# Optimization experiments

Measured on AMD Instinct MI355X. Metric: run time of the kernel, lower is better.

Reference implementation:

```python
import jax, jax.numpy as jnp
import numpy as np

B, T, I, H, G = 4096, 1024, 1, 16, 48  # G = 3*H gates

def _gru_layer(inp, w_ih, w_hh, b_ih, b_hh):
    # inp: [B, T, Din] -> out: [B, T, H]. PyTorch GRU gate math.
    # Precompute all input-side gate projections once (batched GEMM).
    xg = jnp.einsum('btd,gd->tbg', inp, w_ih) + b_ih  # [T, B, 3H]

    def step(h, xg_t):
        hg = h @ w_hh.T + b_hh                         # [B, 3H]
        xr, xz, xn = jnp.split(xg_t, 3, axis=-1)
        hr, hz, hn = jnp.split(hg, 3, axis=-1)
        r = jax.nn.sigmoid(xr + hr)
        z = jax.nn.sigmoid(xz + hz)
        n = jnp.tanh(xn + r * hn)
        h_new = (1.0 - z) * n + z * h
        return h_new, h_new

    h0 = jnp.zeros((inp.shape[0], H), dtype=inp.dtype)
    _, ys = jax.lax.scan(step, h0, xg)                 # ys: [T, B, H]
    return jnp.transpose(ys, (1, 0, 2))                # [B, T, H]

def setup_inputs() -> dict:
    key = jax.random.key(0)
    ks = jax.random.split(key, 8)
    s = 1.0 / np.sqrt(H)  # PyTorch default uniform(-1/sqrt(H), 1/sqrt(H))
    u = lambda k, shape: jax.random.uniform(k, shape, jnp.float32, -s, s)
    return {
        'x':      jax.random.normal(ks[0], (B, T, I), jnp.float32),
        'w_ih0':  u(ks[1], (G, I)),
        'w_ih12': u(ks[2], (2, G, H)),
        'w_hh':   u(ks[3], (3, G, H)),
        'b_ih':   u(ks[4], (3, G)),
        'b_hh':   u(ks[5], (3, G)),
        'fc_w':   u(ks[6], (5, H)),
        'fc_b':   u(ks[7], (5,)),
    }

def reference(x, w_ih0, w_ih12, w_hh, b_ih, b_hh, fc_w, fc_b):
    # 3-layer GRU (dropout=0.3 between layers is identity in eval mode)
    h = _gru_layer(x, w_ih0,     w_hh[0], b_ih[0], b_hh[0])
    h = _gru_layer(h, w_ih12[0], w_hh[1], b_ih[1], b_hh[1])
    h = _gru_layer(h, w_ih12[1], w_hh[2], b_ih[2], b_hh[2])
    # Linear head on the last timestep
    return h[:, -1, :] @ fc_w.T + fc_b                 # [B, 5]
```

## Files before the change

kernel.cpp:

```cpp
#include <hip/hip_runtime.h>
#include <stdint.h>

#define TSTEPS 1024
#define L2E 1.4426950408889634f

typedef float v2f __attribute__((ext_vector_type(2)));
typedef float v4f __attribute__((ext_vector_type(4)));

__device__ __forceinline__ float rcpf_(float v) { return __builtin_amdgcn_rcpf(v); }
__device__ __forceinline__ float ex2(float v) { return __builtin_amdgcn_exp2f(v); }
#define PKFMA(a, b, c) __builtin_elementwise_fma((a), (b), (c))

__device__ __forceinline__ float dpp_x1(float v) {
    return __int_as_float(__builtin_amdgcn_update_dpp(
        0, __float_as_int(v), 0xB1, 0xF, 0xF, true));
}
__device__ __forceinline__ float pairsum(v2f a) {
    float s = a.x + a.y;
    return s + dpp_x1(s);
}

__device__ __forceinline__ v2f ldg2(const float* p) {
    v2f r; uint64_t a = (uint64_t)p;
    asm volatile("global_load_dwordx2 %0, %1, off\n\ts_waitcnt vmcnt(0)"
                 : "=v"(r) : "v"(a));
    return r;
}
__device__ __forceinline__ float ldg1(const float* p) {
    float r; uint64_t a = (uint64_t)p;
    asm volatile("global_load_dword %0, %1, off\n\ts_waitcnt vmcnt(0)"
                 : "=v"(r) : "v"(a));
    return r;
}

__global__ __launch_bounds__(256, 2) void gru3_pair(
    const float* __restrict__ x,
    const float* __restrict__ w_ih0,
    const float* __restrict__ w_ih12,
    const float* __restrict__ w_hh,
    const float* __restrict__ b_ih,
    const float* __restrict__ b_hh,
    const float* __restrict__ fc_w,
    const float* __restrict__ fc_b,
    float* __restrict__ out)
{
    __shared__ float xs[8][TSTEPS];
    __shared__ float hb[8][4][16];

    const int l31 = threadIdx.x & 31;
    const int grp = threadIdx.x >> 5;
    const int u = l31 >> 1;
    const int c = l31 & 1;
    const int c8 = c * 8;
    const int seq = blockIdx.x * 8 + grp;

    {
        const float4* xg = (const float4*)(x + (size_t)blockIdx.x * 8 * TSTEPS);
        float4* xs4 = (float4*)&xs[0][0];
#pragma unroll
        for (int j = 0; j < 8; ++j)
            xs4[threadIdx.x + 256 * j] = xg[threadIdx.x + 256 * j];
        ((float*)hb)[threadIdx.x] = 0.f;
        ((float*)hb)[256 + threadIdx.x] = 0.f;
    }

    const float qs[3] = {-L2E, -L2E, 2.f * L2E};
    v2f wh[3][3][4];
    v2f wi[2][3][4];
#pragma unroll
    for (int l = 0; l < 3; ++l)
#pragma unroll
        for (int q = 0; q < 3; ++q)
#pragma unroll
            for (int m = 0; m < 4; ++m)
                wh[l][q][m] =
                    ldg2(w_hh + (l * 48 + q * 16 + u) * 16 + c8 + 2 * m) * qs[q];
#pragma unroll
    for (int l = 0; l < 2; ++l)
#pragma unroll
        for (int q = 0; q < 3; ++q)
#pragma unroll
            for (int m = 0; m < 4; ++m)
                wi[l][q][m] =
                    ldg2(w_ih12 + (l * 48 + q * 16 + u) * 16 + c8 + 2 * m) * qs[q];

    v2f bir[3], biz[3], binh[3], binx[2];
#pragma unroll
    for (int l = 0; l < 3; ++l) {
        float vr = -(ldg1(b_ih + l * 48 + u) + ldg1(b_hh + l * 48 + u)) * L2E;
        float vz = -(ldg1(b_ih + l * 48 + 16 + u) + ldg1(b_hh + l * 48 + 16 + u)) * L2E;
        float vn = ldg1(b_hh + l * 48 + 32 + u) * (2.f * L2E);
        bir[l] = (v2f){c ? 0.f : vr, 0.f};
        biz[l] = (v2f){c ? 0.f : vz, 0.f};
        binh[l] = (v2f){c ? 0.f : vn, 0.f};
    }
#pragma unroll
    for (int l = 0; l < 2; ++l) {
        float vx = ldg1(b_ih + (l + 1) * 48 + 32 + u) * (2.f * L2E);
        binx[l] = (v2f){c ? 0.f : vx, 0.f};
    }
    const float bnx0 = ldg1(b_ih + 32 + u) * (2.f * L2E);
    const float wxr = ldg1(w_ih0 + u) * -L2E;
    const float wxz = ldg1(w_ih0 + 16 + u) * -L2E;
    const float wxn = ldg1(w_ih0 + 32 + u) * (2.f * L2E);

    __syncthreads();

    v2f h0s[4], h1s[4], h2s[4];
#pragma unroll
    for (int m = 0; m < 4; ++m) {
        h0s[m] = (v2f){0.f, 0.f};
        h1s[m] = (v2f){0.f, 0.f};
        h2s[m] = (v2f){0.f, 0.f};
    }
    float h0o = 0.f, h1o = 0.f, h2o = 0.f;

    const float* xrow = &xs[grp][0];
    float* hw0 = &hb[grp][0][u];
    float* hw1 = &hb[grp][1][u];
    float* hw2 = &hb[grp][2][u];
    const float* hr0 = &hb[grp][0][c8];
    const float* hr1 = &hb[grp][1][c8];
    const float* hr2 = &hb[grp][2][c8];

#define RD4(dst, p)                                                       \
    do {                                                                  \
        v4f ta = *(const v4f*)(p);                                        \
        v4f tb = *(const v4f*)((p) + 4);                                  \
        dst[0] = __builtin_shufflevector(ta, ta, 0, 1);                   \
        dst[1] = __builtin_shufflevector(ta, ta, 2, 3);                   \
        dst[2] = __builtin_shufflevector(tb, tb, 0, 1);                   \
        dst[3] = __builtin_shufflevector(tb, tb, 2, 3);                   \
    } while (0)

    auto step = [&](bool F0, bool F1, bool F2, int t0) {
        v2f a;
        if (F0) {
            float xt = xrow[t0];
            a = PKFMA(wh[0][0][0], h0s[0], bir[0]);
            a = PKFMA(wh[0][0][1], h0s[1], a);
            a = PKFMA(wh[0][0][2], h0s[2], a);
            a = PKFMA(wh[0][0][3], h0s[3], a);
            float sr = fmaf(wxr, xt, pairsum(a));
            a = PKFMA(wh[0][1][0], h0s[0], biz[0]);
            a = PKFMA(wh[0][1][1], h0s[1], a);
            a = PKFMA(wh[0][1][2], h0s[2], a);
            a = PKFMA(wh[0][1][3], h0s[3], a);
            float sz = fmaf(wxz, xt, pairsum(a));
            a = PKFMA(wh[0][2][0], h0s[0], binh[0]);
            a = PKFMA(wh[0][2][1], h0s[1], a);
            a = PKFMA(wh[0][2][2], h0s[2], a);
            a = PKFMA(wh[0][2][3], h0s[3], a);
            float sn = pairsum(a);
            float r = rcpf_(1.f + ex2(sr));
            float z = rcpf_(1.f + ex2(sz));
            float ut = fmaf(r, sn, fmaf(wxn, xt, bnx0));
            float n = fmaf(-2.f, rcpf_(ex2(ut) + 1.f), 1.f);
            h0o = fmaf(z, h0o - n, n);
        }
        if (F1) {
            a = PKFMA(wh[1][0][0], h1s[0], bir[1]);
            a = PKFMA(wh[1][0][1], h1s[1], a);
            a = PKFMA(wh[1][0][2], h1s[2], a);
            a = PKFMA(wh[1][0][3], h1s[3], a);
            a = PKFMA(wi[0][0][0], h0s[0], a);
            a = PKFMA(wi[0][0][1], h0s[1], a);
            a = PKFMA(wi[0][0][2], h0s[2], a);
            a = PKFMA(wi[0][0][3], h0s[3], a);
            float sr = pairsum(a);
            a = PKFMA(wh[1][1][0], h1s[0], biz[1]);
            a = PKFMA(wh[1][1][1], h1s[1], a);
            a = PKFMA(wh[1][1][2], h1s[2], a);
            a = PKFMA(wh[1][1][3], h1s[3], a);
            a = PKFMA(wi[0][1][0], h0s[0], a);
            a = PKFMA(wi[0][1][1], h0s[1], a);
            a = PKFMA(wi[0][1][2], h0s[2], a);
            a = PKFMA(wi[0][1][3], h0s[3], a);
            float sz = pairsum(a);
            a = PKFMA(wh[1][2][0], h1s[0], binh[1]);
            a = PKFMA(wh[1][2][1], h1s[1], a);
            a = PKFMA(wh[1][2][2], h1s[2], a);
            a = PKFMA(wh[1][2][3], h1s[3], a);
            float snh = pairsum(a);
            a = PKFMA(wi[0][2][0], h0s[0], binx[0]);
            a = PKFMA(wi[0][2][1], h0s[1], a);
            a = PKFMA(wi[0][2][2], h0s[2], a);
            a = PKFMA(wi[0][2][3], h0s[3], a);
            float snx = pairsum(a);
            float r = rcpf_(1.f + ex2(sr));
            float z = rcpf_(1.f + ex2(sz));
            float ut = fmaf(r, snh, snx);
            float n = fmaf(-2.f, rcpf_(ex2(ut) + 1.f), 1.f);
            h1o = fmaf(z, h1o - n, n);
        }
        if (F2) {
            a = PKFMA(wh[2][0][0], h2s[0], bir[2]);
            a = PKFMA(wh[2][0][1], h2s[1], a);
            a = PKFMA(wh[2][0][2], h2s[2], a);
            a = PKFMA(wh[2][0][3], h2s[3], a);
            a = PKFMA(wi[1][0][0], h1s[0], a);
            a = PKFMA(wi[1][0][1], h1s[1], a);
            a = PKFMA(wi[1][0][2], h1s[2], a);
            a = PKFMA(wi[1][0][3], h1s[3], a);
            float sr = pairsum(a);
            a = PKFMA(wh[2][1][0], h2s[0], biz[2]);
            a = PKFMA(wh[2][1][1], h2s[1], a);
            a = PKFMA(wh[2][1][2], h2s[2], a);
            a = PKFMA(wh[2][1][3], h2s[3], a);
            a = PKFMA(wi[1][1][0], h1s[0], a);
            a = PKFMA(wi[1][1][1], h1s[1], a);
            a = PKFMA(wi[1][1][2], h1s[2], a);
            a = PKFMA(wi[1][1][3], h1s[3], a);
            float sz = pairsum(a);
            a = PKFMA(wh[2][2][0], h2s[0], binh[2]);
            a = PKFMA(wh[2][2][1], h2s[1], a);
            a = PKFMA(wh[2][2][2], h2s[2], a);
            a = PKFMA(wh[2][2][3], h2s[3], a);
            float snh = pairsum(a);
            a = PKFMA(wi[1][2][0], h1s[0], binx[1]);
            a = PKFMA(wi[1][2][1], h1s[1], a);
            a = PKFMA(wi[1][2][2], h1s[2], a);
            a = PKFMA(wi[1][2][3], h1s[3], a);
            float snx = pairsum(a);
            float r = rcpf_(1.f + ex2(sr));
            float z = rcpf_(1.f + ex2(sz));
            float ut = fmaf(r, snh, snx);
            float n = fmaf(-2.f, rcpf_(ex2(ut) + 1.f), 1.f);
            h2o = fmaf(z, h2o - n, n);
        }
        if (F0) *hw0 = h0o;
        if (F1) *hw1 = h1o;
        if (F2) *hw2 = h2o;
        if (F0) RD4(h0s, hr0);
        if (F1) RD4(h1s, hr1);
        if (F2) RD4(h2s, hr2);
    };

    step(true, false, false, 0);
    step(true, true, false, 1);
#pragma unroll 2
    for (int t0 = 2; t0 < TSTEPS; ++t0) step(true, true, true, t0);
    step(false, true, true, 0);
    step(false, false, true, 0);

    if (l31 < 5) {
        float acc = fc_b[l31];
#pragma unroll
        for (int j = 0; j < 16; ++j)
            acc = fmaf(fc_w[l31 * 16 + j], hb[grp][2][j], acc);
        out[seq * 5 + l31] = acc;
    }
#undef RD4
}

extern "C" void kernel_launch(void* const* d_in, const int* in_sizes, int n_in,
                              void* d_out, int out_size, void* d_ws, size_t ws_size,
                              hipStream_t stream) {
    const float* x      = (const float*)d_in[0];
    const float* w_ih0  = (const float*)d_in[1];
    const float* w_ih12 = (const float*)d_in[2];
    const float* w_hh   = (const float*)d_in[3];
    const float* b_ih   = (const float*)d_in[4];
    const float* b_hh   = (const float*)d_in[5];
    const float* fc_w   = (const float*)d_in[6];
    const float* fc_b   = (const float*)d_in[7];
    float* out = (float*)d_out;

    gru3_pair<<<512, 256, 0, stream>>>(
        x, w_ih0, w_ih12, w_hh, b_ih, b_hh, fc_w, fc_b, out);
}
```

Before: 565.5 us.

## Double-buffer hidden states and split sigmoid work across lane pairs

```diff
diff --git a/kernel.cpp b/kernel.cpp
--- a/kernel.cpp
+++ b/kernel.cpp
@@ -33,7 +33,7 @@
     return r;
 }
 
-__global__ __launch_bounds__(256, 2) void gru3_pair(
+__global__ __launch_bounds__(256, 2) void gru3_pipe(
     const float* __restrict__ x,
     const float* __restrict__ w_ih0,
     const float* __restrict__ w_ih12,
@@ -106,12 +106,12 @@
 
     __syncthreads();
 
-    v2f h0s[4], h1s[4], h2s[4];
+    v2f hA0[4], hA1[4], hA2[4], hB0[4], hB1[4], hB2[4];
 #pragma unroll
     for (int m = 0; m < 4; ++m) {
-        h0s[m] = (v2f){0.f, 0.f};
-        h1s[m] = (v2f){0.f, 0.f};
-        h2s[m] = (v2f){0.f, 0.f};
+        hA0[m] = (v2f){0.f, 0.f};
+        hA1[m] = (v2f){0.f, 0.f};
+        hA2[m] = (v2f){0.f, 0.f};
     }
     float h0o = 0.f, h1o = 0.f, h2o = 0.f;
 
@@ -133,115 +133,127 @@
         dst[3] = __builtin_shufflevector(tb, tb, 2, 3);                   \
     } while (0)
 
-    auto step = [&](bool F0, bool F1, bool F2, int t0) {
-        v2f a;
-        if (F0) {
-            float xt = xrow[t0];
-            a = PKFMA(wh[0][0][0], h0s[0], bir[0]);
-            a = PKFMA(wh[0][0][1], h0s[1], a);
-            a = PKFMA(wh[0][0][2], h0s[2], a);
-            a = PKFMA(wh[0][0][3], h0s[3], a);
-            float sr = fmaf(wxr, xt, pairsum(a));
-            a = PKFMA(wh[0][1][0], h0s[0], biz[0]);
-            a = PKFMA(wh[0][1][1], h0s[1], a);
-            a = PKFMA(wh[0][1][2], h0s[2], a);
-            a = PKFMA(wh[0][1][3], h0s[3], a);
-            float sz = fmaf(wxz, xt, pairsum(a));
-            a = PKFMA(wh[0][2][0], h0s[0], binh[0]);
-            a = PKFMA(wh[0][2][1], h0s[1], a);
-            a = PKFMA(wh[0][2][2], h0s[2], a);
-            a = PKFMA(wh[0][2][3], h0s[3], a);
-            float sn = pairsum(a);
-            float r = rcpf_(1.f + ex2(sr));
-            float z = rcpf_(1.f + ex2(sz));
-            float ut = fmaf(r, sn, fmaf(wxn, xt, bnx0));
-            float n = fmaf(-2.f, rcpf_(ex2(ut) + 1.f), 1.f);
-            h0o = fmaf(z, h0o - n, n);
-        }
-        if (F1) {
-            a = PKFMA(wh[1][0][0], h1s[0], bir[1]);
-            a = PKFMA(wh[1][0][1], h1s[1], a);
-            a = PKFMA(wh[1][0][2], h1s[2], a);
-            a = PKFMA(wh[1][0][3], h1s[3], a);
-            a = PKFMA(wi[0][0][0], h0s[0], a);
-            a = PKFMA(wi[0][0][1], h0s[1], a);
-            a = PKFMA(wi[0][0][2], h0s[2], a);
-            a = PKFMA(wi[0][0][3], h0s[3], a);
-            float sr = pairsum(a);
-            a = PKFMA(wh[1][1][0], h1s[0], biz[1]);
-            a = PKFMA(wh[1][1][1], h1s[1], a);
-            a = PKFMA(wh[1][1][2], h1s[2], a);
-            a = PKFMA(wh[1][1][3], h1s[3], a);
-            a = PKFMA(wi[0][1][0], h0s[0], a);
-            a = PKFMA(wi[0][1][1], h0s[1], a);
-            a = PKFMA(wi[0][1][2], h0s[2], a);
-            a = PKFMA(wi[0][1][3], h0s[3], a);
-            float sz = pairsum(a);
-            a = PKFMA(wh[1][2][0], h1s[0], binh[1]);
-            a = PKFMA(wh[1][2][1], h1s[1], a);
-            a = PKFMA(wh[1][2][2], h1s[2], a);
-            a = PKFMA(wh[1][2][3], h1s[3], a);
-            float snh = pairsum(a);
-            a = PKFMA(wi[0][2][0], h0s[0], binx[0]);
-            a = PKFMA(wi[0][2][1], h0s[1], a);
-            a = PKFMA(wi[0][2][2], h0s[2], a);
-            a = PKFMA(wi[0][2][3], h0s[3], a);
-            float snx = pairsum(a);
-            float r = rcpf_(1.f + ex2(sr));
-            float z = rcpf_(1.f + ex2(sz));
-            float ut = fmaf(r, snh, snx);
-            float n = fmaf(-2.f, rcpf_(ex2(ut) + 1.f), 1.f);
-            h1o = fmaf(z, h1o - n, n);
-        }
-        if (F2) {
-            a = PKFMA(wh[2][0][0], h2s[0], bir[2]);
-            a = PKFMA(wh[2][0][1], h2s[1], a);
-            a = PKFMA(wh[2][0][2], h2s[2], a);
-            a = PKFMA(wh[2][0][3], h2s[3], a);
-            a = PKFMA(wi[1][0][0], h1s[0], a);
-            a = PKFMA(wi[1][0][1], h1s[1], a);
-            a = PKFMA(wi[1][0][2], h1s[2], a);
-            a = PKFMA(wi[1][0][3], h1s[3], a);
-            float sr = pairsum(a);
-            a = PKFMA(wh[2][1][0], h2s[0], biz[2]);
-            a = PKFMA(wh[2][1][1], h2s[1], a);
-            a = PKFMA(wh[2][1][2], h2s[2], a);
-            a = PKFMA(wh[2][1][3], h2s[3], a);
-            a = PKFMA(wi[1][1][0], h1s[0], a);
-            a = PKFMA(wi[1][1][1], h1s[1], a);
-            a = PKFMA(wi[1][1][2], h1s[2], a);
-            a = PKFMA(wi[1][1][3], h1s[3], a);
-            float sz = pairsum(a);
-            a = PKFMA(wh[2][2][0], h2s[0], binh[2]);
-            a = PKFMA(wh[2][2][1], h2s[1], a);
-            a = PKFMA(wh[2][2][2], h2s[2], a);
-            a = PKFMA(wh[2][2][3], h2s[3], a);
-            float snh = pairsum(a);
-            a = PKFMA(wi[1][2][0], h1s[0], binx[1]);
-            a = PKFMA(wi[1][2][1], h1s[1], a);
-            a = PKFMA(wi[1][2][2], h1s[2], a);
-            a = PKFMA(wi[1][2][3], h1s[3], a);
-            float snx = pairsum(a);
-            float r = rcpf_(1.f + ex2(sr));
-            float z = rcpf_(1.f + ex2(sz));
-            float ut = fmaf(r, snh, snx);
-            float n = fmaf(-2.f, rcpf_(ex2(ut) + 1.f), 1.f);
-            h2o = fmaf(z, h2o - n, n);
-        }
-        if (F0) *hw0 = h0o;
-        if (F1) *hw1 = h1o;
-        if (F2) *hw2 = h2o;
-        if (F0) RD4(h0s, hr0);
-        if (F1) RD4(h1s, hr1);
-        if (F2) RD4(h2s, hr2);
-    };
-
-    step(true, false, false, 0);
-    step(true, true, false, 1);
-#pragma unroll 2
-    for (int t0 = 2; t0 < TSTEPS; ++t0) step(true, true, true, t0);
-    step(false, true, true, 0);
-    step(false, false, true, 0);
+#define STEP(I0, I1, I2, O0, O1, O2, F0, F1, F2, XT)                      \
+  do {                                                                    \
+    v2f a;                                                                \
+    if (F0) {                                                             \
+      a = PKFMA(wh[0][0][0], I0[0], bir[0]);                              \
+      a = PKFMA(wh[0][0][1], I0[1], a);                                   \
+      a = PKFMA(wh[0][0][2], I0[2], a);                                   \
+      a = PKFMA(wh[0][0][3], I0[3], a);                                   \
+      float sr = fmaf(wxr, (XT), pairsum(a));                             \
+      a = PKFMA(wh[0][1][0], I0[0], biz[0]);                              \
+      a = PKFMA(wh[0][1][1], I0[1], a);                                   \
+      a = PKFMA(wh[0][1][2], I0[2], a);                                   \
+      a = PKFMA(wh[0][1][3], I0[3], a);                                   \
+      float sz = fmaf(wxz, (XT), pairsum(a));                             \
+      a = PKFMA(wh[0][2][0], I0[0], binh[0]);                             \
+      a = PKFMA(wh[0][2][1], I0[1], a);                                   \
+      a = PKFMA(wh[0][2][2], I0[2], a);                                   \
+      a = PKFMA(wh[0][2][3], I0[3], a);                                   \
+      float sn = pairsum(a);                                              \
+      float p = c ? sz : sr;                                              \
+      float sg = rcpf_(1.f + ex2(p));                                     \
+      float og = dpp_x1(sg);                                              \
+      float r = c ? og : sg;                                              \
+      float z = c ? sg : og;                                              \
+      float ut = fmaf(r, sn, fmaf(wxn, (XT), bnx0));                      \
+      float n = fmaf(-2.f, rcpf_(ex2(ut) + 1.f), 1.f);                    \
+      h0o = fmaf(z, h0o - n, n);                                          \
+    }                                                                     \
+    *hw0 = h0o;                                                           \
+    RD4(O0, hr0);                                                         \
+    if (F1) {                                                             \
+      a = PKFMA(wh[1][0][0], I1[0], bir[1]);                              \
+      a = PKFMA(wh[1][0][1], I1[1], a);                                   \
+      a = PKFMA(wh[1][0][2], I1[2], a);                                   \
+      a = PKFMA(wh[1][0][3], I1[3], a);                                   \
+      a = PKFMA(wi[0][0][0], I0[0], a);                                   \
+      a = PKFMA(wi[0][0][1], I0[1], a);                                   \
+      a = PKFMA(wi[0][0][2], I0[2], a);                                   \
+      a = PKFMA(wi[0][0][3], I0[3], a);                                   \
+      float sr = pairsum(a);                                              \
+      a = PKFMA(wh[1][1][0], I1[0], biz[1]);                              \
+      a = PKFMA(wh[1][1][1], I1[1], a);                                   \
+      a = PKFMA(wh[1][1][2], I1[2], a);                                   \
+      a = PKFMA(wh[1][1][3], I1[3], a);                                   \
+      a = PKFMA(wi[0][1][0], I0[0], a);                                   \
+      a = PKFMA(wi[0][1][1], I0[1], a);                                   \
+      a = PKFMA(wi[0][1][2], I0[2], a);                                   \
+      a = PKFMA(wi[0][1][3], I0[3], a);                                   \
+      float sz = pairsum(a);                                              \
+      a = PKFMA(wh[1][2][0], I1[0], binh[1]);                             \
+      a = PKFMA(wh[1][2][1], I1[1], a);                                   \
+      a = PKFMA(wh[1][2][2], I1[2], a);                                   \
+      a = PKFMA(wh[1][2][3], I1[3], a);                                   \
+      float snh = pairsum(a);                                             \
+      a = PKFMA(wi[0][2][0], I0[0], binx[0]);                             \
+      a = PKFMA(wi[0][2][1], I0[1], a);                                   \
+      a = PKFMA(wi[0][2][2], I0[2], a);                                   \
+      a = PKFMA(wi[0][2][3], I0[3], a);                                   \
+      float snx = pairsum(a);                                             \
+      float p = c ? sz : sr;                                              \
+      float sg = rcpf_(1.f + ex2(p));                                     \
+      float og = dpp_x1(sg);                                              \
+      float r = c ? og : sg;                                              \
+      float z = c ? sg : og;                                              \
+      float ut = fmaf(r, snh, snx);                                       \
+      float n = fmaf(-2.f, rcpf_(ex2(ut) + 1.f), 1.f);                    \
+      h1o = fmaf(z, h1o - n, n);                                          \
+    }                                                                     \
+    *hw1 = h1o;                                                           \
+    RD4(O1, hr1);                                                         \
+    if (F2) {                                                             \
+      a = PKFMA(wh[2][0][0], I2[0], bir[2]);                              \
+      a = PKFMA(wh[2][0][1], I2[1], a);                                   \
+      a = PKFMA(wh[2][0][2], I2[2], a);                                   \
+      a = PKFMA(wh[2][0][3], I2[3], a);                                   \
+      a = PKFMA(wi[1][0][0], I1[0], a);                                   \
+      a = PKFMA(wi[1][0][1], I1[1], a);                                   \
+      a = PKFMA(wi[1][0][2], I1[2], a);                                   \
+      a = PKFMA(wi[1][0][3], I1[3], a);                                   \
+      float sr = pairsum(a);                                              \
+      a = PKFMA(wh[2][1][0], I2[0], biz[2]);                              \
+      a = PKFMA(wh[2][1][1], I2[1], a);                                   \
+      a = PKFMA(wh[2][1][2], I2[2], a);                                   \
+      a = PKFMA(wh[2][1][3], I2[3], a);                                   \
+      a = PKFMA(wi[1][1][0], I1[0], a);                                   \
+      a = PKFMA(wi[1][1][1], I1[1], a);                                   \
+      a = PKFMA(wi[1][1][2], I1[2], a);                                   \
+      a = PKFMA(wi[1][1][3], I1[3], a);                                   \
+      float sz = pairsum(a);                                              \
+      a = PKFMA(wh[2][2][0], I2[0], binh[2]);                             \
+      a = PKFMA(wh[2][2][1], I2[1], a);                                   \
+      a = PKFMA(wh[2][2][2], I2[2], a);                                   \
+      a = PKFMA(wh[2][2][3], I2[3], a);                                   \
+      float snh = pairsum(a);                                             \
+      a = PKFMA(wi[1][2][0], I1[0], binx[1]);                             \
+      a = PKFMA(wi[1][2][1], I1[1], a);                                   \
+      a = PKFMA(wi[1][2][2], I1[2], a);                                   \
+      a = PKFMA(wi[1][2][3], I1[3], a);                                   \
+      float snx = pairsum(a);                                             \
+      float p = c ? sz : sr;                                              \
+      float sg = rcpf_(1.f + ex2(p));                                     \
+      float og = dpp_x1(sg);                                              \
+      float r = c ? og : sg;                                              \
+      float z = c ? sg : og;                                              \
+      float ut = fmaf(r, snh, snx);                                       \
+      float n = fmaf(-2.f, rcpf_(ex2(ut) + 1.f), 1.f);                    \
+      h2o = fmaf(z, h2o - n, n);                                          \
+    }                                                                     \
+    *hw2 = h2o;                                                           \
+    RD4(O2, hr2);                                                         \
+  } while (0)
+
+    STEP(hA0, hA1, hA2, hB0, hB1, hB2, true, false, false, xrow[0]);
+    STEP(hB0, hB1, hB2, hA0, hA1, hA2, true, true, false, xrow[1]);
+    for (int t0 = 2; t0 < TSTEPS; t0 += 2) {
+        v2f x2 = *(const v2f*)&xrow[t0];
+        STEP(hA0, hA1, hA2, hB0, hB1, hB2, true, true, true, x2.x);
+        STEP(hB0, hB1, hB2, hA0, hA1, hA2, true, true, true, x2.y);
+    }
+    STEP(hA0, hA1, hA2, hB0, hB1, hB2, false, true, true, 0.f);
+    STEP(hB0, hB1, hB2, hA0, hA1, hA2, false, false, true, 0.f);
 
     if (l31 < 5) {
         float acc = fc_b[l31];
@@ -251,6 +263,7 @@
         out[seq * 5 + l31] = acc;
     }
 #undef RD4
+#undef STEP
 }
 
 extern "C" void kernel_launch(void* const* d_in, const int* in_sizes, int n_in,
@@ -266,6 +279,6 @@
     const float* fc_b   = (const float*)d_in[7];
     float* out = (float*)d_out;
 
-    gru3_pair<<<512, 256, 0, stream>>>(
+    gru3_pipe<<<512, 256, 0, stream>>>(
         x, w_ih0, w_ih12, w_hh, b_ih, b_hh, fc_w, fc_b, out);
 }
```

Measured after the change: 570.3 us. Within noise of the previous version (+0.8%).

## Split gate nonlinearities across lane pairs to halve per-lane transcendental work

Applied to the files above, without the earlier changes.

```diff
diff --git a/kernel.cpp b/kernel.cpp
--- a/kernel.cpp
+++ b/kernel.cpp
@@ -33,7 +33,11 @@
     return r;
 }
 
-__global__ __launch_bounds__(256, 2) void gru3_pair(
+#define CH4(W, H, SEED) \
+    PKFMA(W[3], H[3], PKFMA(W[2], H[2], PKFMA(W[1], H[1], PKFMA(W[0], H[0], (SEED)))))
+#define CH8(Wa, Ha, Wb, Hb, SEED) CH4(Wa, Ha, CH4(Wb, Hb, (SEED)))
+
+__global__ __launch_bounds__(256, 2) void gru3_tp(
     const float* __restrict__ x,
     const float* __restrict__ w_ih0,
     const float* __restrict__ w_ih12,
@@ -113,11 +117,11 @@
         h1s[m] = (v2f){0.f, 0.f};
         h2s[m] = (v2f){0.f, 0.f};
     }
-    float h0o = 0.f, h1o = 0.f, h2o = 0.f;
+    float h01o = 0.f;
+    float h2o = 0.f;
 
     const float* xrow = &xs[grp][0];
-    float* hw0 = &hb[grp][0][u];
-    float* hw1 = &hb[grp][1][u];
+    float* hw01 = &hb[grp][c][u];
     float* hw2 = &hb[grp][2][u];
     const float* hr0 = &hb[grp][0][c8];
     const float* hr1 = &hb[grp][1][c8];
@@ -133,115 +137,71 @@
         dst[3] = __builtin_shufflevector(tb, tb, 2, 3);                   \
     } while (0)
 
-    auto step = [&](bool F0, bool F1, bool F2, int t0) {
-        v2f a;
+    auto step = [&](bool F0, bool F1, bool F2, float xt) {
+        float sg0 = 0.f, og0 = 0.f, sg1 = 0.f, og1 = 0.f;
+        float snh0 = 0.f, snx0 = 0.f, snh1 = 0.f, snx1 = 0.f;
         if (F0) {
-            float xt = xrow[t0];
-            a = PKFMA(wh[0][0][0], h0s[0], bir[0]);
-            a = PKFMA(wh[0][0][1], h0s[1], a);
-            a = PKFMA(wh[0][0][2], h0s[2], a);
-            a = PKFMA(wh[0][0][3], h0s[3], a);
-            float sr = fmaf(wxr, xt, pairsum(a));
-            a = PKFMA(wh[0][1][0], h0s[0], biz[0]);
-            a = PKFMA(wh[0][1][1], h0s[1], a);
-            a = PKFMA(wh[0][1][2], h0s[2], a);
-            a = PKFMA(wh[0][1][3], h0s[3], a);
-            float sz = fmaf(wxz, xt, pairsum(a));
-            a = PKFMA(wh[0][2][0], h0s[0], binh[0]);
-            a = PKFMA(wh[0][2][1], h0s[1], a);
-            a = PKFMA(wh[0][2][2], h0s[2], a);
-            a = PKFMA(wh[0][2][3], h0s[3], a);
-            float sn = pairsum(a);
-            float r = rcpf_(1.f + ex2(sr));
-            float z = rcpf_(1.f + ex2(sz));
-            float ut = fmaf(r, sn, fmaf(wxn, xt, bnx0));
+            float sr = fmaf(wxr, xt, pairsum(CH4(wh[0][0], h0s, bir[0])));
+            float sz = fmaf(wxz, xt, pairsum(CH4(wh[0][1], h0s, biz[0])));
+            float p = c ? sz : sr;
+            sg0 = rcpf_(1.f + ex2(p));
+            og0 = dpp_x1(sg0);
+            snh0 = pairsum(CH4(wh[0][2], h0s, binh[0]));
+            snx0 = fmaf(wxn, xt, bnx0);
+        }
+        if (F1) {
+            float sr = pairsum(CH8(wh[1][0], h1s, wi[0][0], h0s, bir[1]));
+            float sz = pairsum(CH8(wh[1][1], h1s, wi[0][1], h0s, biz[1]));
+            float p = c ? sz : sr;
+            sg1 = rcpf_(1.f + ex2(p));
+            og1 = dpp_x1(sg1);
+            snh1 = pairsum(CH4(wh[1][2], h1s, binh[1]));
+            snx1 = pairsum(CH4(wi[0][2], h0s, binx[0]));
+        }
+        if (F0 || F1) {
+            float rsel = c ? og1 : sg0;
+            float zsel = c ? sg1 : og0;
+            float snh = c ? snh1 : snh0;
+            float snx = c ? snx1 : snx0;
+            float ut = fmaf(rsel, snh, snx);
             float n = fmaf(-2.f, rcpf_(ex2(ut) + 1.f), 1.f);
-            h0o = fmaf(z, h0o - n, n);
-        }
-        if (F1) {
-            a = PKFMA(wh[1][0][0], h1s[0], bir[1]);
-            a = PKFMA(wh[1][0][1], h1s[1], a);
-            a = PKFMA(wh[1][0][2], h1s[2], a);
-            a = PKFMA(wh[1][0][3], h1s[3], a);
-            a = PKFMA(wi[0][0][0], h0s[0], a);
-            a = PKFMA(wi[0][0][1], h0s[1], a);
-            a = PKFMA(wi[0][0][2], h0s[2], a);
-            a = PKFMA(wi[0][0][3], h0s[3], a);
-            float sr = pairsum(a);
-            a = PKFMA(wh[1][1][0], h1s[0], biz[1]);
-            a = PKFMA(wh[1][1][1], h1s[1], a);
-            a = PKFMA(wh[1][1][2], h1s[2], a);
-            a = PKFMA(wh[1][1][3], h1s[3], a);
-            a = PKFMA(wi[0][1][0], h0s[0], a);
-            a = PKFMA(wi[0][1][1], h0s[1], a);
-            a = PKFMA(wi[0][1][2], h0s[2], a);
-            a = PKFMA(wi[0][1][3], h0s[3], a);
-            float sz = pairsum(a);
-            a = PKFMA(wh[1][2][0], h1s[0], binh[1]);
-            a = PKFMA(wh[1][2][1], h1s[1], a);
-            a = PKFMA(wh[1][2][2], h1s[2], a);
-            a = PKFMA(wh[1][2][3], h1s[3], a);
-            float snh = pairsum(a);
-            a = PKFMA(wi[0][2][0], h0s[0], binx[0]);
-            a = PKFMA(wi[0][2][1], h0s[1], a);
-            a = PKFMA(wi[0][2][2], h0s[2], a);
-            a = PKFMA(wi[0][2][3], h0s[3], a);
-            float snx = pairsum(a);
-            float r = rcpf_(1.f + ex2(sr));
-            float z = rcpf_(1.f + ex2(sz));
-            float ut = fmaf(r, snh, snx);
+            float hn = fmaf(zsel, h01o - n, n);
+            bool act = c ? F1 : F0;
+            h01o = act ? hn : h01o;
+        }
+        *hw01 = h01o;
+        if (F2) {
+            float sr = pairsum(CH8(wh[2][0], h2s, wi[1][0], h1s, bir[2]));
+            float sz = pairsum(CH8(wh[2][1], h2s, wi[1][1], h1s, biz[2]));
+            float p = c ? sz : sr;
+            float sg = rcpf_(1.f + ex2(p));
+            float og = dpp_x1(sg);
+            float r2 = c ? og : sg;
+            float z2 = c ? sg : og;
+            float snh = pairsum(CH4(wh[2][2], h2s, binh[2]));
+            float snx = pairsum(CH4(wi[1][2], h1s, binx[1]));
+            float ut = fmaf(r2, snh, snx);
             float n = fmaf(-2.f, rcpf_(ex2(ut) + 1.f), 1.f);
-            h1o = fmaf(z, h1o - n, n);
-        }
-        if (F2) {
-            a = PKFMA(wh[2][0][0], h2s[0], bir[2]);
-            a = PKFMA(wh[2][0][1], h2s[1], a);
-            a = PKFMA(wh[2][0][2], h2s[2], a);
-            a = PKFMA(wh[2][0][3], h2s[3], a);
-            a = PKFMA(wi[1][0][0], h1s[0], a);
-            a = PKFMA(wi[1][0][1], h1s[1], a);
-            a = PKFMA(wi[1][0][2], h1s[2], a);
-            a = PKFMA(wi[1][0][3], h1s[3], a);
-            float sr = pairsum(a);
-            a = PKFMA(wh[2][1][0], h2s[0], biz[2]);
-            a = PKFMA(wh[2][1][1], h2s[1], a);
-            a = PKFMA(wh[2][1][2], h2s[2], a);
-            a = PKFMA(wh[2][1][3], h2s[3], a);
-            a = PKFMA(wi[1][1][0], h1s[0], a);
-            a = PKFMA(wi[1][1][1], h1s[1], a);
-            a = PKFMA(wi[1][1][2], h1s[2], a);
-            a = PKFMA(wi[1][1][3], h1s[3], a);
-            float sz = pairsum(a);
-            a = PKFMA(wh[2][2][0], h2s[0], binh[2]);
-            a = PKFMA(wh[2][2][1], h2s[1], a);
-            a = PKFMA(wh[2][2][2], h2s[2], a);
-            a = PKFMA(wh[2][2][3], h2s[3], a);
-            float snh = pairsum(a);
-            a = PKFMA(wi[1][2][0], h1s[0], binx[1]);
-            a = PKFMA(wi[1][2][1], h1s[1], a);
-            a = PKFMA(wi[1][2][2], h1s[2], a);
-            a = PKFMA(wi[1][2][3], h1s[3], a);
-            float snx = pairsum(a);
-            float r = rcpf_(1.f + ex2(sr));
-            float z = rcpf_(1.f + ex2(sz));
-            float ut = fmaf(r, snh, snx);
-            float n = fmaf(-2.f, rcpf_(ex2(ut) + 1.f), 1.f);
-            h2o = fmaf(z, h2o - n, n);
-        }
-        if (F0) *hw0 = h0o;
-        if (F1) *hw1 = h1o;
-        if (F2) *hw2 = h2o;
-        if (F0) RD4(h0s, hr0);
-        if (F1) RD4(h1s, hr1);
-        if (F2) RD4(h2s, hr2);
+            h2o = fmaf(z2, h2o - n, n);
+        }
+        *hw2 = h2o;
+        RD4(h0s, hr0);
+        RD4(h1s, hr1);
+        RD4(h2s, hr2);
     };
 
-    step(true, false, false, 0);
-    step(true, true, false, 1);
-#pragma unroll 2
-    for (int t0 = 2; t0 < TSTEPS; ++t0) step(true, true, true, t0);
-    step(false, true, true, 0);
-    step(false, false, true, 0);
+    v2f xc = *(const v2f*)&xrow[0];
+    step(true, false, false, xc.x);
+    step(true, true, false, xc.y);
+    v2f xn = *(const v2f*)&xrow[2];
+    for (int t0 = 2; t0 < TSTEPS; t0 += 2) {
+        xc = xn;
+        xn = *(const v2f*)&xrow[(t0 + 2) & (TSTEPS - 1)];
+        step(true, true, true, xc.x);
+        step(true, true, true, xc.y);
+    }
+    step(false, true, true, 0.f);
+    step(false, false, true, 0.f);
 
     if (l31 < 5) {
         float acc = fc_b[l31];
@@ -266,6 +226,6 @@
     const float* fc_b   = (const float*)d_in[7];
     float* out = (float*)d_out;
 
-    gru3_pair<<<512, 256, 0, stream>>>(
+    gru3_tp<<<512, 256, 0, stream>>>(
         x, w_ih0, w_ih12, w_hh, b_ih, b_hh, fc_w, fc_b, out);
 }
```

New measurement: 540.4 us. 4.4% less time.
